# Kernel tuning notes

Measured on AMD Instinct MI355X. Metric: run time of the kernel, lower is better.

## Reference

```python
import jax, jax.numpy as jnp
import numpy as np

K = 20
BN_EPS = 1e-5


def setup_inputs() -> dict:
    key = jax.random.key(0)
    ks = jax.random.split(key, 6)
    B, N, H = 2, 4096, 384
    s = lambda k, sh, sc: jax.random.normal(k, sh, dtype=jnp.float32) * sc
    return {
        "xyz": jax.random.normal(ks[0], (B, N, 3), dtype=jnp.float32),
        "W1": s(ks[1], (6, 128), 0.2),   "b1": jnp.zeros((128,), jnp.float32),
        "g1": jnp.ones((128,), jnp.float32), "be1": jnp.zeros((128,), jnp.float32),
        "W2": s(ks[2], (128, 256), 0.08), "b2": jnp.zeros((256,), jnp.float32),
        "W3": s(ks[3], (512, 512), 0.05), "b3": jnp.zeros((512,), jnp.float32),
        "g3": jnp.ones((512,), jnp.float32), "be3": jnp.zeros((512,), jnp.float32),
        "W4": s(ks[4], (512, H), 0.05),  "b4": jnp.zeros((H,), jnp.float32),
    }


def _knn_idx(x, k):
    # x: [B,N,3] -> k nearest neighbor indices (incl. self), sorted by distance
    sq = jnp.sum(x * x, axis=-1)                                  # [B,N]
    d2 = sq[:, :, None] + sq[:, None, :] - 2.0 * jnp.einsum('bnd,bmd->bnm', x, x)
    _, idx = jax.lax.top_k(-d2, k)                                # [B,N,k]
    return jax.lax.stop_gradient(idx)


def _bn_relu(h, gamma, beta):
    # BatchNorm1d in training mode: per-channel stats over (batch, length) dims.
    # h: [M, k, C]
    mu = jnp.mean(h, axis=(0, 1), keepdims=True)
    var = jnp.var(h, axis=(0, 1), keepdims=True)  # biased, matches torch BN
    return jax.nn.relu((h - mu) * jax.lax.rsqrt(var + BN_EPS) * gamma + beta)


def reference(xyz, W1, b1, g1, be1, W2, b2, W3, b3, g3, be3, W4, b4):
    B, N, _ = xyz.shape
    idx = _knn_idx(xyz, K)                                        # [B,N,K]
    nbr = jax.vmap(lambda pts, i: pts[i])(xyz, idx)               # [B,N,K,3]
    ctr = xyz[:, :, None, :]
    edge = jnp.concatenate([nbr - ctr, jnp.broadcast_to(ctr, nbr.shape)], axis=-1)
    h = edge.reshape(B * N, K, 6)                                 # [M,K,6]
    # conv1: Conv1d(6,128) -> BN -> ReLU -> Conv1d(128,256)  (kernel-1 convs == matmul)
    h = _bn_relu(h @ W1 + b1, g1, be1)
    h = h @ W2 + b2                                               # [M,K,256]
    gmax = jnp.max(h, axis=1, keepdims=True)                      # [M,1,256]
    f = jnp.concatenate([jnp.broadcast_to(gmax, h.shape), h], axis=-1)  # [M,K,512]
    # conv2: Conv1d(512,512) -> BN -> ReLU -> Conv1d(512,hidden)
    f = _bn_relu(f @ W3 + b3, g3, be3)
    f = f @ W4 + b4                                               # [M,K,H]
    feature = jnp.max(f, axis=1).reshape(B, N, -1)                # [B,N,H]
    return (xyz, feature)
```

## Files before the change

kernel.cpp:

```cpp
#include <hip/hip_runtime.h>
#include <float.h>

#define NPTS_B 4096
#define NPTS 8192
#define KNN 20
#define NSAMP (NPTS*KNN)

typedef __attribute__((ext_vector_type(8))) short bf16x8;
typedef __attribute__((ext_vector_type(4))) float f32x4;

static __device__ __forceinline__ float bf2f(unsigned short u) {
  return __uint_as_float(((unsigned int)u) << 16);
}
static __device__ __forceinline__ unsigned short f2bf(float f) {
  unsigned int u = __float_as_uint(f);
  u += 0x7fffu + ((u >> 16) & 1u);
  return (unsigned short)(u >> 16);
}
static __device__ __forceinline__ void gl_lds16(const void* g, void* l) {
  __builtin_amdgcn_global_load_lds(
      (const __attribute__((address_space(1))) unsigned int*)g,
      (__attribute__((address_space(3))) unsigned int*)l, 16, 0, 0);
}

__global__ __launch_bounds__(256) void wprep_kernel(const float* __restrict__ W3,
                                                    const float* __restrict__ W4,
                                                    const float* __restrict__ W2,
                                                    unsigned short* __restrict__ W3T,
                                                    unsigned short* __restrict__ W4T,
                                                    unsigned short* __restrict__ W2T) {
  int id = blockIdx.x * 256 + threadIdx.x;
  if (id < 512*512) {
    int n = id >> 9, k = id & 511;
    W3T[id] = f2bf(W3[k*512 + n]);
  } else if (id < 512*512 + 384*512) {
    int id2 = id - 512*512;
    int n = id2 >> 9, k = id2 & 511;
    W4T[id2] = f2bf(W4[k*384 + n]);
  } else {
    int id2 = id - (512*512 + 384*512);
    int n = id2 >> 7, k = id2 & 127;
    W2T[id2] = f2bf(W2[k*256 + n]);
  }
}

__global__ __launch_bounds__(256) void xyzprep_kernel(const float* __restrict__ xyz,
                                                      float* __restrict__ xT) {
#pragma clang fp contract(off)
  int j = blockIdx.x * 256 + threadIdx.x;
  int b = j >> 12, jj = j & 4095;
  float x = xyz[j*3+0], y = xyz[j*3+1], z = xyz[j*3+2];
  float sq = (x*x + y*y) + z*z;
  float* base = xT + (size_t)b*16384;
  base[jj] = x; base[4096+jj] = y; base[8192+jj] = z; base[12288+jj] = sq;
}

__global__ __launch_bounds__(256) void knn_kernel(const float* __restrict__ xyz,
                                                  const float* __restrict__ xT,
                                                  int* __restrict__ idx,
                                                  float* __restrict__ out_xyz) {
#pragma clang fp contract(off)
  int p = blockIdx.x;
  int b = p >> 12;
  int base = b << 12;
  int tid = threadIdx.x;
  const float* xb = xT + (size_t)b*16384;
  float xi0 = xyz[p*3+0], xi1 = xyz[p*3+1], xi2 = xyz[p*3+2];
  float sqi = (xi0*xi0 + xi1*xi1) + xi2*xi2;

  __shared__ __align__(16) int hist[4096];
  __shared__ int sL1[256];
  __shared__ int nsel, binB;

#pragma unroll
  for (int u = 0; u < 16; ++u) hist[tid + (u << 8)] = 0;
  if (tid == 0) nsel = 0;
  __syncthreads();

  unsigned long long cand[16];
#pragma unroll
  for (int u = 0; u < 16; ++u) {
    int j = tid + (u << 8);
    float a0 = xb[j], a1 = xb[4096 + j], a2 = xb[8192 + j];
    float sqj = xb[12288 + j];
    float dt  = (xi0*a0 + xi1*a1) + xi2*a2;
    float d2  = (sqi + sqj) - 2.0f*dt;
    unsigned int kb = __float_as_uint(d2);
    cand[u] = ((unsigned long long)kb << 32) | (unsigned int)j;
    atomicAdd(&hist[kb >> 20], 1);
  }
  __syncthreads();

  {
    int s = 0;
#pragma unroll
    for (int u = 0; u < 16; ++u) s += hist[tid*16 + u];
    sL1[tid] = s;
  }
  __syncthreads();

  if (tid < 64) {
    int v = sL1[tid*4] + sL1[tid*4+1] + sL1[tid*4+2] + sL1[tid*4+3];
    int incl = v;
#pragma unroll
    for (int off = 1; off < 64; off <<= 1) {
      int t = __shfl_up(incl, off);
      if (tid >= off) incl += t;
    }
    unsigned long long ball = __ballot(incl >= KNN);
    int L = __ffsll(ball) - 1;
    if (tid == L) {
      int cum = incl - v;
      int bfound = -1;
      for (int t2 = 4*L; t2 < 4*L + 4; ++t2) {
        int s = sL1[t2];
        if (bfound < 0) {
          if (cum + s >= KNN) {
            for (int u = 0; u < 16; ++u) {
              int c = hist[t2*16 + u];
              if (cum + c >= KNN) { bfound = t2*16 + u; break; }
              cum += c;
            }
          } else {
            cum += s;
          }
        }
      }
      binB = bfound;
    }
  }
  __syncthreads();

  int B = binB;
  unsigned long long* list = (unsigned long long*)hist;
#pragma unroll
  for (int u = 0; u < 16; ++u) {
    if ((int)(unsigned int)(cand[u] >> 52) <= B) {
      int pos = atomicAdd(&nsel, 1);
      if (pos < 2048) list[pos] = cand[u];
    }
  }
  __syncthreads();

  int n = nsel; if (n > 2048) n = 2048;
  for (int t = tid; t < n; t += 256) {
    unsigned long long me = list[t];
    int rank = 0;
    for (int i = 0; i < n; ++i) rank += (list[i] < me);
    if (rank < KNN) idx[p*20 + rank] = base + (int)(me & 0xffffffffu);
  }
  if (tid < 3) out_xyz[p*3 + tid] = xyz[p*3 + tid];
}

__global__ __launch_bounds__(256) void h1_moments_kernel(const float* __restrict__ xyz,
                                                         const int* __restrict__ idx,
                                                         float* __restrict__ mbuck) {
  int tid = threadIdx.x, blk = blockIdx.x;
  float A[33] = {};
#pragma unroll
  for (int u = 0; u < 2; ++u) {
    int s = blk*512 + (u << 8) + tid;
    unsigned int p = (unsigned int)s / 20u;
    int jg = idx[s];
    float c0 = xyz[p*3+0], c1 = xyz[p*3+1], c2 = xyz[p*3+2];
    float e[6];
    e[0] = xyz[jg*3+0] - c0; e[1] = xyz[jg*3+1] - c1; e[2] = xyz[jg*3+2] - c2;
    e[3] = c0; e[4] = c1; e[5] = c2;
    int k = 6;
#pragma unroll
    for (int d = 0; d < 6; ++d) {
      A[d] += e[d];
#pragma unroll
      for (int d2 = d; d2 < 6; ++d2) { A[k] = fmaf(e[d], e[d2], A[k]); ++k; }
    }
  }
#pragma unroll
  for (int off = 1; off < 64; off <<= 1) {
#pragma unroll
    for (int i = 0; i < 33; ++i) A[i] += __shfl_xor(A[i], off);
  }
  if ((tid & 63) == 0) {
    int b = ((blk << 2) | (tid >> 6)) & 15;
    for (int i = 0; i < 33; ++i) atomicAdd(&mbuck[b*64 + i], A[i]);
  }
}

__global__ void bn_prep1(const float* __restrict__ W1, const float* __restrict__ b1,
                         const float* __restrict__ g1, const float* __restrict__ be1,
                         const float* __restrict__ mbuck, float* __restrict__ misc) {
  __shared__ float red[33];
  int tid = threadIdx.x;
  if (tid < 33) {
    float s = 0.f;
    for (int b = 0; b < 16; ++b) s += mbuck[b*64 + tid];
    red[tid] = s;
  }
  __syncthreads();
  int c = tid;
  float w[6];
#pragma unroll
  for (int d = 0; d < 6; ++d) w[d] = W1[d*128 + c];
  const float inv = 1.0f / (float)NSAMP;
  float t = 0.f;
#pragma unroll
  for (int d = 0; d < 6; ++d) t = fmaf(w[d], red[d], t);
  t *= inv;
  float Q = 0.f;
  int k = 6;
#pragma unroll
  for (int d = 0; d < 6; ++d) {
#pragma unroll
    for (int d2 = d; d2 < 6; ++d2) {
      float coef = (d == d2) ? w[d]*w[d] : 2.f*w[d]*w[d2];
      Q = fmaf(coef, red[k], Q); ++k;
    }
  }
  Q *= inv;
  float var = Q - t*t;
  float mu = b1[c] + t;
  float a = g1[c] / sqrtf(var + 1e-5f);
  misc[c] = a;
  misc[128 + c] = be1[c] - mu*a;
}

__global__ __launch_bounds__(256) void h2_kernel(const float* __restrict__ xyz,
                                                 const int* __restrict__ idx,
                                                 const float* __restrict__ W1,
                                                 const float* __restrict__ b1,
                                                 const unsigned short* __restrict__ W2T,
                                                 const float* __restrict__ b2,
                                                 const float* __restrict__ misc,
                                                 unsigned short* __restrict__ h2out,
                                                 unsigned short* __restrict__ gmaxout) {
  int p0 = blockIdx.x << 2;
  int tid = threadIdx.x;
  int w = tid >> 6, lane = tid & 63;
  int lr = lane & 15, lg = lane >> 4;
  __shared__ __align__(16) char smem[42240];
  float (*e)[6] = (float (*)[6])smem;
  unsigned short (*As)[136] = (unsigned short (*)[136])(smem + 1920);
  unsigned short (*Cs)[264] = (unsigned short (*)[264])smem;

  bf16x8 bfr[4][4];
#pragma unroll
  for (int j = 0; j < 4; ++j)
#pragma unroll
    for (int kk = 0; kk < 4; ++kk)
      bfr[j][kk] = *(const bf16x8*)(W2T + (size_t)(w*64 + j*16 + lr)*128 + kk*32 + lg*8);

  if (tid < 80) {
    int pl = (unsigned int)tid / 20u;
    int p = p0 + pl;
    int jg = idx[p0*20 + tid];
    float xi0 = xyz[p*3+0], xi1 = xyz[p*3+1], xi2 = xyz[p*3+2];
    e[tid][0] = xyz[jg*3+0] - xi0;
    e[tid][1] = xyz[jg*3+1] - xi1;
    e[tid][2] = xyz[jg*3+2] - xi2;
    e[tid][3] = xi0; e[tid][4] = xi1; e[tid][5] = xi2;
  }
  __syncthreads();

  {
    int c = tid & 127, half = tid >> 7;
    float w1v[6];
#pragma unroll
    for (int d = 0; d < 6; ++d) w1v[d] = W1[d*128 + c];
    float b1v = b1[c], a1 = misc[c], d1 = misc[128 + c];
#pragma unroll
    for (int u = 0; u < 40; ++u) {
      int row = (u << 1) | half;
      float v = b1v;
#pragma unroll
      for (int d = 0; d < 6; ++d) v = fmaf(e[row][d], w1v[d], v);
      v = fmaxf(fmaf(a1, v, d1), 0.f);
      As[row][c] = f2bf(v);
    }
  }
  __syncthreads();

  f32x4 acc[5][4] = {};
#pragma unroll
  for (int kk = 0; kk < 4; ++kk) {
    bf16x8 a[5];
#pragma unroll
    for (int i = 0; i < 5; ++i)
      a[i] = *(const bf16x8*)&As[i*16 + lr][kk*32 + lg*8];
#pragma unroll
    for (int i = 0; i < 5; ++i)
#pragma unroll
      for (int j = 0; j < 4; ++j)
        acc[i][j] = __builtin_amdgcn_mfma_f32_16x16x32_bf16(a[i], bfr[j][kk], acc[i][j], 0, 0, 0);
  }
  __syncthreads();

  float b2v[4];
#pragma unroll
  for (int j = 0; j < 4; ++j) b2v[j] = b2[w*64 + j*16 + lr];
#pragma unroll
  for (int i = 0; i < 5; ++i)
#pragma unroll
    for (int j = 0; j < 4; ++j) {
      int col = w*64 + j*16 + lr;
#pragma unroll
      for (int r = 0; r < 4; ++r)
        Cs[i*16 + lg*4 + r][col] = f2bf(acc[i][j][r] + b2v[j]);
    }
  __syncthreads();

#pragma unroll
  for (int l = 0; l < 10; ++l) {
    int id = tid + (l << 8);
    int row = id >> 5, chk = id & 31;
    *(uint4*)(h2out + (size_t)(p0*20 + row)*256 + (chk << 3)) =
        *(const uint4*)&Cs[row][chk << 3];
  }
#pragma unroll
  for (int l = 0; l < 4; ++l) {
    int id = tid + (l << 8);
    int q = id >> 8, col = id & 255;
    float v = bf2f(Cs[q*20][col]);
#pragma unroll
    for (int u = 1; u < 20; ++u) v = fmaxf(v, bf2f(Cs[q*20 + u][col]));
    gmaxout[(size_t)(p0 + q)*256 + col] = f2bf(v);
  }
}

__global__ __launch_bounds__(256) void pgemm_kernel(const unsigned short* __restrict__ gmax,
                                                    const unsigned short* __restrict__ W3T,
                                                    unsigned short* __restrict__ Pg) {
  int bid = blockIdx.x;
  int bm = bid >> 1, bn = bid & 1;
  int m0 = bm << 6, n0 = bn << 8;
  int tid = threadIdx.x;
  int lane = tid & 63, w = tid >> 6;
  int lr = lane & 15, lg = lane >> 4;
  __shared__ __align__(16) char smem[40960];
  unsigned short (*As)[64] = (unsigned short (*)[64])smem;
  unsigned short (*Bs)[64] = (unsigned short (*)[64])(smem + 8192);
  unsigned short (*Cs)[264] = (unsigned short (*)[264])smem;

  int swz = lr >> 1;
  f32x4 acc[4][4] = {};
  for (int kc = 0; kc < 256; kc += 64) {
#pragma unroll
    for (int l = 0; l < 2; ++l) {
      int id = tid + (l << 8);
      int row = id >> 3, ks = id & 7, kg = ks ^ ((id >> 4) & 7);
      gl_lds16(gmax + (size_t)(m0 + row)*256 + kc + (kg << 3), &As[row][ks << 3]);
    }
#pragma unroll
    for (int l = 0; l < 8; ++l) {
      int id = tid + (l << 8);
      int row = id >> 3, ks = id & 7, kg = ks ^ ((id >> 4) & 7);
      gl_lds16(W3T + (size_t)(n0 + row)*512 + kc + (kg << 3), &Bs[row][ks << 3]);
    }
    __syncthreads();
#pragma unroll
    for (int h = 0; h < 2; ++h) {
      int ch = ((h << 2) | lg) ^ swz;
      bf16x8 a[4], b[4];
#pragma unroll
      for (int t = 0; t < 4; ++t)
        a[t] = *(const bf16x8*)&As[t*16 + lr][ch << 3];
#pragma unroll
      for (int t = 0; t < 4; ++t)
        b[t] = *(const bf16x8*)&Bs[w*64 + t*16 + lr][ch << 3];
#pragma unroll
      for (int i = 0; i < 4; ++i)
#pragma unroll
        for (int j = 0; j < 4; ++j)
          acc[i][j] = __builtin_amdgcn_mfma_f32_16x16x32_bf16(a[i], b[j], acc[i][j], 0, 0, 0);
    }
    __syncthreads();
  }
#pragma unroll
  for (int i = 0; i < 4; ++i)
#pragma unroll
    for (int j = 0; j < 4; ++j)
#pragma unroll
      for (int r = 0; r < 4; ++r)
        Cs[i*16 + lg*4 + r][w*64 + j*16 + lr] = f2bf(acc[i][j][r]);
  __syncthreads();
#pragma unroll
  for (int l = 0; l < 8; ++l) {
    int id = tid + (l << 8);
    int row = id >> 5, chk = id & 31;
    *(uint4*)(Pg + (size_t)(m0 + row)*512 + n0 + (chk << 3)) =
        *(const uint4*)&Cs[row][chk << 3];
  }
}

__global__ __launch_bounds__(512, 4) void gemm3_kernel(const unsigned short* __restrict__ h2,
                                                       const unsigned short* __restrict__ Pg,
                                                       const unsigned short* __restrict__ W3T,
                                                       const float* __restrict__ b3,
                                                       unsigned short* __restrict__ h3,
                                                       float* __restrict__ s3buck) {
  int bid = blockIdx.x;
  int grp = bid >> 4, rem = bid & 15;
  int bn = rem >> 3;
  int bm = (grp << 3) | (rem & 7);
  int m0 = bm << 7, n0 = bn << 8;
  int tid = threadIdx.x;
  int lane = tid & 63, w = tid >> 6;
  int mw = w >> 2, nw = w & 3;
  int lr = lane & 15, lg = lane >> 4;
  __shared__ __align__(16) char smem[35840];
  unsigned short (*As)[32] = (unsigned short (*)[32])smem;
  unsigned short (*Bs)[32] = (unsigned short (*)[32])(smem + 8192);
  unsigned short (*Cs)[264] = (unsigned short (*)[264])smem;
  float* ssum = (float*)(smem + 33792);
  float* ssq  = ssum + 256;

  int arow = tid >> 2, aks = tid & 3, akg = aks ^ ((tid >> 3) & 3);

  int ch = (lg ^ ((lr >> 1) & 3)) << 3;

  f32x4 acc[4][4] = {};
  for (int t = 0; t < 8; ++t) {
    int kc = t << 5;
    gl_lds16(h2 + (size_t)(m0 + arow)*256 + kc + (akg << 3),
             &As[arow][aks << 3]);
#pragma unroll
    for (int l = 0; l < 2; ++l) {
      int id = tid + (l << 9);
      int brow = id >> 2, bks = id & 3, bkg = bks ^ ((id >> 3) & 3);
      gl_lds16(W3T + (size_t)(n0 + brow)*512 + 256 + kc + (bkg << 3),
               &Bs[brow][bks << 3]);
    }
    __syncthreads();
    bf16x8 a[4], b[4];
#pragma unroll
    for (int i = 0; i < 4; ++i)
      a[i] = *(const bf16x8*)&As[mw*64 + i*16 + lr][ch];
#pragma unroll
    for (int j = 0; j < 4; ++j)
      b[j] = *(const bf16x8*)&Bs[nw*64 + j*16 + lr][ch];
#pragma unroll
    for (int i = 0; i < 4; ++i)
#pragma unroll
      for (int j = 0; j < 4; ++j)
        acc[i][j] = __builtin_amdgcn_mfma_f32_16x16x32_bf16(a[i], b[j], acc[i][j], 0, 0, 0);
    __syncthreads();
  }

  if (tid < 256) { ssum[tid] = 0.f; ssq[tid] = 0.f; }
  __syncthreads();
  unsigned int pt[4][4];
#pragma unroll
  for (int i = 0; i < 4; ++i) {
    int rbase = m0 + mw*64 + i*16 + lg*4;
#pragma unroll
    for (int r = 0; r < 4; ++r)
      pt[i][r] = (unsigned int)(rbase + r) / 20u;
  }
#pragma unroll
  for (int half = 0; half < 2; ++half) {
    if (mw == half) {
#pragma unroll
      for (int j = 0; j < 4; ++j) {
        int colL = nw*64 + j*16 + lr;
        float b3v = b3[n0 + colL];
        float sumv = 0.f, sqv = 0.f;
#pragma unroll
        for (int i = 0; i < 4; ++i) {
#pragma unroll
          for (int r = 0; r < 4; ++r) {
            float v = acc[i][j][r] + b3v +
                      bf2f(Pg[(size_t)pt[i][r]*512 + n0 + colL]);
            Cs[i*16 + lg*4 + r][colL] = f2bf(v);
            sumv += v; sqv = fmaf(v, v, sqv);
          }
        }
        sumv += __shfl_xor(sumv, 16); sumv += __shfl_xor(sumv, 32);
        sqv  += __shfl_xor(sqv, 16);  sqv  += __shfl_xor(sqv, 32);
        if (lg == 0) {
          atomicAdd(&ssum[colL], sumv);
          atomicAdd(&ssq[colL], sqv);
        }
      }
    }
    __syncthreads();
#pragma unroll
    for (int l = 0; l < 4; ++l) {
      int id = tid + (l << 9);
      int row = id >> 5, chk = id & 31;
      *(uint4*)(h3 + (size_t)(m0 + half*64 + row)*512 + n0 + (chk << 3)) =
          *(const uint4*)&Cs[row][chk << 3];
    }
    __syncthreads();
  }
  if (tid < 256) {
    int bkt = (bid & 63) * 1024;
    atomicAdd(&s3buck[bkt + n0 + tid], ssum[tid]);
    atomicAdd(&s3buck[bkt + 512 + n0 + tid], ssq[tid]);
  }
}

__global__ void bn_prep3(const float* __restrict__ g3, const float* __restrict__ be3,
                         const float* __restrict__ s3buck, float* __restrict__ misc) {
  int c = threadIdx.x;
  float s = 0.f, q = 0.f;
  for (int b = 0; b < 64; ++b) { s += s3buck[b*1024 + c]; q += s3buck[b*1024 + 512 + c]; }
  const float inv = 1.0f / (float)NSAMP;
  float mu = s * inv;
  float var = q * inv - mu * mu;
  float a = g3[c] / sqrtf(var + 1e-5f);
  misc[256 + c] = a;
  misc[768 + c] = be3[c] - mu * a;
}

__global__ __launch_bounds__(512, 4) void gemm4_kernel(const unsigned short* __restrict__ h3,
                                                       const unsigned short* __restrict__ W4T,
                                                       const float* __restrict__ b4,
                                                       const float* __restrict__ misc,
                                                       float* __restrict__ outf) {
  int bm = blockIdx.x;
  int m0 = bm * 80;
  int tid = threadIdx.x;
  int lane = tid & 63, w = tid >> 6;
  int lr = lane & 15, lg = lane >> 4;
  __shared__ __align__(16) char smem[63488];
  unsigned short (*As)[64] = (unsigned short (*)[64])smem;
  unsigned short (*Bs)[64] = (unsigned short (*)[64])(smem + 10240);
  float (*pool)[392] = (float (*)[392])smem;
  float* af = (float*)(smem + 59392);
  float* df = af + 512;
  if (tid < 512) {
    af[tid] = misc[256 + tid];
    df[tid] = misc[768 + tid];
  }
  __syncthreads();
  f32x4 acc[5][3] = {};

  int arow = tid >> 3, aks = tid & 7, akg = aks ^ ((tid >> 4) & 7);
  uint4 aR0, aR1;
  aR0 = *(const uint4*)(h3 + (size_t)(m0 + arow)*512 + (akg << 3));
  if (tid < 128)
    aR1 = *(const uint4*)(h3 + (size_t)(m0 + 64 + arow)*512 + (akg << 3));

  for (int kc = 0; kc < 512; kc += 64) {
#pragma unroll
    for (int l = 0; l < 6; ++l) {
      int id = tid + (l << 9);
      int row = id >> 3, ks = id & 7, kg = ks ^ ((id >> 4) & 7);
      gl_lds16(W4T + (size_t)row*512 + kc + (kg << 3), &Bs[row][ks << 3]);
    }
    {
      int k0 = kc + (akg << 3);
      unsigned int o[4];
#pragma unroll
      for (int q = 0; q < 4; ++q) {
        unsigned int u = ((const unsigned int*)&aR0)[q];
        float lo = bf2f((unsigned short)(u & 0xffffu));
        float hi = bf2f((unsigned short)(u >> 16));
        lo = fmaxf(fmaf(af[k0 + q*2],     lo, df[k0 + q*2]),     0.f);
        hi = fmaxf(fmaf(af[k0 + q*2 + 1], hi, df[k0 + q*2 + 1]), 0.f);
        o[q] = (unsigned int)f2bf(lo) | ((unsigned int)f2bf(hi) << 16);
      }
      *(uint4*)&As[arow][aks << 3] = *(const uint4*)o;
      if (tid < 128) {
        unsigned int o1[4];
#pragma unroll
        for (int q = 0; q < 4; ++q) {
          unsigned int u = ((const unsigned int*)&aR1)[q];
          float lo = bf2f((unsigned short)(u & 0xffffu));
          float hi = bf2f((unsigned short)(u >> 16));
          lo = fmaxf(fmaf(af[k0 + q*2],     lo, df[k0 + q*2]),     0.f);
          hi = fmaxf(fmaf(af[k0 + q*2 + 1], hi, df[k0 + q*2 + 1]), 0.f);
          o1[q] = (unsigned int)f2bf(lo) | ((unsigned int)f2bf(hi) << 16);
        }
        *(uint4*)&As[64 + arow][aks << 3] = *(const uint4*)o1;
      }
    }
    __syncthreads();
    int kn = kc + 64;
    if (kn < 512) {
      aR0 = *(const uint4*)(h3 + (size_t)(m0 + arow)*512 + kn + (akg << 3));
      if (tid < 128)
        aR1 = *(const uint4*)(h3 + (size_t)(m0 + 64 + arow)*512 + kn + (akg << 3));
    }
#pragma unroll
    for (int h = 0; h < 2; ++h) {
      int ch = ((h << 2) | lg) ^ (lr >> 1);
      bf16x8 a[5], b[3];
#pragma unroll
      for (int t = 0; t < 5; ++t)
        a[t] = *(const bf16x8*)&As[t*16 + lr][ch << 3];
#pragma unroll
      for (int t = 0; t < 3; ++t)
        b[t] = *(const bf16x8*)&Bs[w*48 + t*16 + lr][ch << 3];
#pragma unroll
      for (int i = 0; i < 5; ++i)
#pragma unroll
        for (int j = 0; j < 3; ++j)
          acc[i][j] = __builtin_amdgcn_mfma_f32_16x16x32_bf16(a[i], b[j], acc[i][j], 0, 0, 0);
    }
    __syncthreads();
  }

#pragma unroll
  for (int i = 0; i < 5; ++i)
#pragma unroll
    for (int j = 0; j < 3; ++j) {
      float m = fmaxf(fmaxf(acc[i][j][0], acc[i][j][1]),
                      fmaxf(acc[i][j][2], acc[i][j][3]));
      pool[i*4 + lg][w*48 + j*16 + lr] = m;
    }
  __syncthreads();
#pragma unroll
  for (int l = 0; l < 3; ++l) {
    int id = tid + (l << 9);
    int q = id / 384, c = id - q*384;
    float v = pool[q*5][c];
#pragma unroll
    for (int u = 1; u < 5; ++u) v = fmaxf(v, pool[q*5 + u][c]);
    outf[(size_t)(bm*4 + q)*384 + c] = v + b4[c];
  }
}

extern "C" void kernel_launch(void* const* d_in, const int* in_sizes, int n_in,
                              void* d_out, int out_size, void* d_ws, size_t ws_size,
                              hipStream_t stream) {
  const float* xyz = (const float*)d_in[0];
  const float* W1  = (const float*)d_in[1];
  const float* b1  = (const float*)d_in[2];
  const float* g1  = (const float*)d_in[3];
  const float* be1 = (const float*)d_in[4];
  const float* W2  = (const float*)d_in[5];
  const float* b2  = (const float*)d_in[6];
  const float* W3  = (const float*)d_in[7];
  const float* b3  = (const float*)d_in[8];
  const float* g3  = (const float*)d_in[9];
  const float* be3 = (const float*)d_in[10];
  const float* W4  = (const float*)d_in[11];
  const float* b4  = (const float*)d_in[12];

  char* ws = (char*)d_ws;
  int*            idx    = (int*)ws;
  float*          misc   = (float*)(ws + 0xA0000);
  float*          mbuck  = (float*)(ws + 0xA2000);
  float*          s3buck = (float*)(ws + 0xAA000);
  unsigned short* W3T    = (unsigned short*)(ws + 0xF0000);
  unsigned short* W4T    = (unsigned short*)(ws + 0x170000);
  unsigned short* W2T    = (unsigned short*)(ws + 0x1D0000);
  unsigned short* gmax   = (unsigned short*)(ws + 0x200000);
  unsigned short* h2     = (unsigned short*)(ws + 0x600000);
  unsigned short* h3     = (unsigned short*)(ws + 0x5600000ULL);
  unsigned short* Pg     = (unsigned short*)(ws + 0xF600000ULL);
  float*          xT     = (float*)(ws + 0xFE00000ULL);

  float* ofp   = (float*)d_out;
  float* oxyz  = ofp;
  float* ofeat = ofp + 24576;

  hipMemsetAsync(ws + 0xA2000, 0, 0x48000, stream);

  wprep_kernel<<<(512*512 + 384*512 + 256*128)/256, 256, 0, stream>>>(W3, W4, W2, W3T, W4T, W2T);
  xyzprep_kernel<<<NPTS/256, 256, 0, stream>>>(xyz, xT);
  knn_kernel<<<NPTS, 256, 0, stream>>>(xyz, xT, idx, oxyz);
  h1_moments_kernel<<<NSAMP/512, 256, 0, stream>>>(xyz, idx, mbuck);
  bn_prep1<<<1, 128, 0, stream>>>(W1, b1, g1, be1, mbuck, misc);
  h2_kernel<<<NPTS/4, 256, 0, stream>>>(xyz, idx, W1, b1, W2T, b2, misc, h2, gmax);
  pgemm_kernel<<<256, 256, 0, stream>>>(gmax, W3T, Pg);
  gemm3_kernel<<<(NSAMP/128)*2, 512, 0, stream>>>(h2, Pg, W3T, b3, h3, s3buck);
  bn_prep3<<<1, 512, 0, stream>>>(g3, be3, s3buck, misc);
  gemm4_kernel<<<NPTS/4, 512, 0, stream>>>(h3, W4T, b4, misc, ofeat);
}
```

Measured before the change: 354.9 us.

## Enlarge gemm3 tile to 256x256 with 1024 threads and 64-wide K chunks

The gemm3 kernel now uses 256-row by 256-column tiles with 16 waves per block, and loads 64-wide K slices per iteration instead of 32, using an 8-way XOR swizzle. This halves the number of K-loop barriers and improves reuse of A and B tiles, so less global traffic is needed per output. The grouped block-index remap for L2 locality is dropped. The cost is larger LDS use (about 66KB) and fewer, bigger blocks, which may reduce occupancy and latency hiding.

```diff
diff --git a/kernel.cpp b/kernel.cpp
--- a/kernel.cpp
+++ b/kernel.cpp
@@ -390,57 +390,63 @@
   }
 }
 
-__global__ __launch_bounds__(512, 4) void gemm3_kernel(const unsigned short* __restrict__ h2,
-                                                       const unsigned short* __restrict__ Pg,
-                                                       const unsigned short* __restrict__ W3T,
-                                                       const float* __restrict__ b3,
-                                                       unsigned short* __restrict__ h3,
-                                                       float* __restrict__ s3buck) {
+__global__ __launch_bounds__(1024, 4) void gemm3_kernel(const unsigned short* __restrict__ h2,
+                                                        const unsigned short* __restrict__ Pg,
+                                                        const unsigned short* __restrict__ W3T,
+                                                        const float* __restrict__ b3,
+                                                        unsigned short* __restrict__ h3,
+                                                        float* __restrict__ s3buck) {
   int bid = blockIdx.x;
-  int grp = bid >> 4, rem = bid & 15;
-  int bn = rem >> 3;
-  int bm = (grp << 3) | (rem & 7);
-  int m0 = bm << 7, n0 = bn << 8;
+  int bm = bid >> 1, bn = bid & 1;
+  int m0 = bm << 8, n0 = bn << 8;
   int tid = threadIdx.x;
   int lane = tid & 63, w = tid >> 6;
   int mw = w >> 2, nw = w & 3;
   int lr = lane & 15, lg = lane >> 4;
-  __shared__ __align__(16) char smem[35840];
-  unsigned short (*As)[32] = (unsigned short (*)[32])smem;
-  unsigned short (*Bs)[32] = (unsigned short (*)[32])(smem + 8192);
+  __shared__ __align__(16) char smem[67584];
+  unsigned short (*As)[64] = (unsigned short (*)[64])smem;
+  unsigned short (*Bs)[64] = (unsigned short (*)[64])(smem + 32768);
+  float* ssum = (float*)(smem + 65536);
+  float* ssq  = ssum + 256;
   unsigned short (*Cs)[264] = (unsigned short (*)[264])smem;
-  float* ssum = (float*)(smem + 33792);
-  float* ssq  = ssum + 256;
-
-  int arow = tid >> 2, aks = tid & 3, akg = aks ^ ((tid >> 3) & 3);
-
-  int ch = (lg ^ ((lr >> 1) & 3)) << 3;
+
+  int rS[2], ksS[2], kgS[2];
+#pragma unroll
+  for (int l = 0; l < 2; ++l) {
+    int id = tid + (l << 10);
+    rS[l] = id >> 3;
+    ksS[l] = id & 7;
+    kgS[l] = ksS[l] ^ ((id >> 4) & 7);
+  }
+  int swz = lr >> 1;
 
   f32x4 acc[4][4] = {};
-  for (int t = 0; t < 8; ++t) {
-    int kc = t << 5;
-    gl_lds16(h2 + (size_t)(m0 + arow)*256 + kc + (akg << 3),
-             &As[arow][aks << 3]);
-#pragma unroll
-    for (int l = 0; l < 2; ++l) {
-      int id = tid + (l << 9);
-      int brow = id >> 2, bks = id & 3, bkg = bks ^ ((id >> 3) & 3);
-      gl_lds16(W3T + (size_t)(n0 + brow)*512 + 256 + kc + (bkg << 3),
-               &Bs[brow][bks << 3]);
-    }
-    __syncthreads();
-    bf16x8 a[4], b[4];
-#pragma unroll
-    for (int i = 0; i < 4; ++i)
-      a[i] = *(const bf16x8*)&As[mw*64 + i*16 + lr][ch];
-#pragma unroll
-    for (int j = 0; j < 4; ++j)
-      b[j] = *(const bf16x8*)&Bs[nw*64 + j*16 + lr][ch];
-#pragma unroll
-    for (int i = 0; i < 4; ++i)
-#pragma unroll
-      for (int j = 0; j < 4; ++j)
-        acc[i][j] = __builtin_amdgcn_mfma_f32_16x16x32_bf16(a[i], b[j], acc[i][j], 0, 0, 0);
+  for (int kc = 0; kc < 256; kc += 64) {
+#pragma unroll
+    for (int l = 0; l < 2; ++l)
+      gl_lds16(h2 + (size_t)(m0 + rS[l])*256 + kc + (kgS[l] << 3),
+               &As[rS[l]][ksS[l] << 3]);
+#pragma unroll
+    for (int l = 0; l < 2; ++l)
+      gl_lds16(W3T + (size_t)(n0 + rS[l])*512 + 256 + kc + (kgS[l] << 3),
+               &Bs[rS[l]][ksS[l] << 3]);
+    __syncthreads();
+#pragma unroll
+    for (int h = 0; h < 2; ++h) {
+      int ch = ((h << 2) | lg) ^ swz;
+      bf16x8 a[4], b[4];
+#pragma unroll
+      for (int t = 0; t < 4; ++t)
+        a[t] = *(const bf16x8*)&As[mw*64 + t*16 + lr][ch << 3];
+#pragma unroll
+      for (int t = 0; t < 4; ++t)
+        b[t] = *(const bf16x8*)&Bs[nw*64 + t*16 + lr][ch << 3];
+#pragma unroll
+      for (int i = 0; i < 4; ++i)
+#pragma unroll
+        for (int j = 0; j < 4; ++j)
+          acc[i][j] = __builtin_amdgcn_mfma_f32_16x16x32_bf16(a[i], b[j], acc[i][j], 0, 0, 0);
+    }
     __syncthreads();
   }
 
@@ -455,8 +461,8 @@
       pt[i][r] = (unsigned int)(rbase + r) / 20u;
   }
 #pragma unroll
-  for (int half = 0; half < 2; ++half) {
-    if (mw == half) {
+  for (int q = 0; q < 4; ++q) {
+    if (mw == q) {
 #pragma unroll
       for (int j = 0; j < 4; ++j) {
         int colL = nw*64 + j*16 + lr;
@@ -482,10 +488,10 @@
     }
     __syncthreads();
 #pragma unroll
-    for (int l = 0; l < 4; ++l) {
-      int id = tid + (l << 9);
+    for (int l = 0; l < 2; ++l) {
+      int id = tid + (l << 10);
       int row = id >> 5, chk = id & 31;
-      *(uint4*)(h3 + (size_t)(m0 + half*64 + row)*512 + n0 + (chk << 3)) =
+      *(uint4*)(h3 + (size_t)(m0 + q*64 + row)*512 + n0 + (chk << 3)) =
           *(const uint4*)&Cs[row][chk << 3];
     }
     __syncthreads();
@@ -663,7 +669,7 @@
   bn_prep1<<<1, 128, 0, stream>>>(W1, b1, g1, be1, mbuck, misc);
   h2_kernel<<<NPTS/4, 256, 0, stream>>>(xyz, idx, W1, b1, W2T, b2, misc, h2, gmax);
   pgemm_kernel<<<256, 256, 0, stream>>>(gmax, W3T, Pg);
-  gemm3_kernel<<<(NSAMP/128)*2, 512, 0, stream>>>(h2, Pg, W3T, b3, h3, s3buck);
+  gemm3_kernel<<<(NSAMP/256)*2, 1024, 0, stream>>>(h2, Pg, W3T, b3, h3, s3buck);
   bn_prep3<<<1, 512, 0, stream>>>(g3, be3, s3buck, misc);
   gemm4_kernel<<<NPTS/4, 512, 0, stream>>>(h3, W4T, b4, misc, ofeat);
 }
```

Result: slower. 379.6 us (+7.0%).
